# Kernel optimization log

Measured on AMD Instinct MI355X. Metric: run time of the kernel, lower is better.

The kernel has to match this reference:

```python
import jax, jax.numpy as jnp
import numpy as np
import math

B, T, I, H = 16, 16384, 1, 64
OS = 48000.0 / 44100.0  # os_factor


def setup_inputs() -> dict:
    key = jax.random.key(0)
    k0, k1, k2, k3, k4 = jax.random.split(key, 5)
    s = 1.0 / math.sqrt(H)  # torch LSTMCell init range
    x = jax.random.normal(k0, (B, T, I), dtype=jnp.float32)
    W_ih = jax.random.uniform(k1, (4 * H, I), minval=-s, maxval=s, dtype=jnp.float32)
    W_hh = jax.random.uniform(k2, (4 * H, H), minval=-s, maxval=s, dtype=jnp.float32)
    b_ih = jax.random.uniform(k3, (4 * H,), minval=-s, maxval=s, dtype=jnp.float32)
    b_hh = jax.random.uniform(k4, (4 * H,), minval=-s, maxval=s, dtype=jnp.float32)
    return {"x": x, "W_ih": W_ih, "W_hh": W_hh, "b_ih": b_ih, "b_hh": b_hh}


def reference(x, W_ih, W_hh, b_ih, b_hh):
    # allpass fractional-delay parameters (static, os_factor in [1, 2))
    delay_near = math.floor(OS)          # = 1
    alpha = OS - delay_near
    ap_coeff = (1.0 - alpha) / (1.0 + alpha)
    Bsz = x.shape[0]
    S = 2 * H  # LSTM state_size = cat(h, c)

    def lstm_cell(xi, hc):
        h, c = hc[:, :H], hc[:, H:]
        gates = xi @ W_ih.T + b_ih + h @ W_hh.T + b_hh  # [B, 4H]
        ig, fg, gg, og = jnp.split(gates, 4, axis=-1)
        ig = jax.nn.sigmoid(ig)
        fg = jax.nn.sigmoid(fg)
        gg = jnp.tanh(gg)
        og = jax.nn.sigmoid(og)
        c_new = fg * c + ig * gg
        h_new = og * jnp.tanh(c_new)
        return jnp.concatenate([h_new, c_new], axis=-1)  # [B, 2H]

    zeros = jnp.zeros((Bsz, S), dtype=x.dtype)

    def step(carry, xi):
        ap, s1, s2 = carry  # s1 = states[i-1], s2 = states[i-2] (zeros before start)
        ap = ap_coeff * (s1 - ap) + s2
        hc = lstm_cell(xi, ap)
        return (ap, hc, s1), hc

    xs = jnp.swapaxes(x, 0, 1)  # [T, B, I]
    (ap_final, _, _), states = jax.lax.scan(step, (zeros, zeros, zeros), xs)
    states = jnp.swapaxes(states, 0, 1)  # [B, T, 2H]
    y = states[..., :H]
    return y, states[..., H:], ap_final
```

## Files before the change

### kernel.cpp

```cpp
#include <hip/hip_runtime.h>

#define Hdim 64
#define Tlen 16384
#define Bsz  16
#define LOG2E 1.44269504088896340736f

__device__ __forceinline__ float rlane(float v, int l) {
    return __int_as_float(__builtin_amdgcn_readlane(__float_as_int(v), l));
}

__device__ __forceinline__ float sigm(float x) {
    return __builtin_amdgcn_rcpf(1.0f + __builtin_amdgcn_exp2f(-LOG2E * x));
}
__device__ __forceinline__ float tanhfast(float x) {
    const float e = __builtin_amdgcn_exp2f((2.0f * LOG2E) * x);
    return fmaf(-2.0f, __builtin_amdgcn_rcpf(e + 1.0f), 1.0f);
}

__global__ void __launch_bounds__(256, 1)
apdl_rnn_kernel(const float* __restrict__ x,
                const float* __restrict__ W_ih,
                const float* __restrict__ W_hh,
                const float* __restrict__ b_ih,
                const float* __restrict__ b_hh,
                float* __restrict__ out)
{
    const int b    = blockIdx.x;
    const int tid  = threadIdx.x;
    const int wid  = tid >> 6;
    const int lane = tid & 63;

    float w[Hdim];
    #pragma unroll
    for (int k = 0; k < Hdim; k += 4) {
        const float4 v = *reinterpret_cast<const float4*>(&W_hh[tid * Hdim + k]);
        w[k] = v.x; w[k + 1] = v.y; w[k + 2] = v.z; w[k + 3] = v.w;
    }
    const float bias = b_ih[tid] + b_hh[tid];
    const float wih  = W_ih[tid];

    const float apc = 0.8375f;

    float ap_h = 0.f, ap_c = 0.f;
    float h1 = 0.f, c1 = 0.f;
    float h2 = 0.f, c2 = 0.f;

    __shared__ float gbuf[2][256];
    __shared__ float apbuf[4][Hdim];

    const float* xb = x + (size_t)b * Tlen;
    float xnext = xb[lane];
    float xcur  = 0.f;

    float* yp = out + (size_t)b * Tlen * Hdim + lane;
    float* cp = out + (size_t)Bsz * Tlen * Hdim + (size_t)b * Tlen * Hdim + lane;

    float* apw = &apbuf[wid][0];

    for (int t = 0; t < Tlen; ++t) {
        #pragma unroll
        for (int k = 0; k < Hdim; k += 4) {
            asm volatile("" : "+v"(w[k]), "+v"(w[k+1]), "+v"(w[k+2]), "+v"(w[k+3]));
        }

        if ((t & 63) == 0) {
            xcur = xnext;
            if (t + 64 < Tlen) xnext = xb[t + 64 + lane];
        }
        const float xt = rlane(xcur, t & 63);

        ap_h = fmaf(apc, h1 - ap_h, h2);
        ap_c = fmaf(apc, c1 - ap_c, c2);

        apw[lane] = ap_h;

        float a0 = fmaf(xt, wih, bias);
        float a1 = 0.f, a2 = 0.f, a3 = 0.f;
        const float4* hp = reinterpret_cast<const float4*>(apw);
        #pragma unroll
        for (int k4 = 0; k4 < Hdim / 4; ++k4) {
            const float4 hv = hp[k4];
            a0 = fmaf(hv.x, w[4 * k4    ], a0);
            a1 = fmaf(hv.y, w[4 * k4 + 1], a1);
            a2 = fmaf(hv.z, w[4 * k4 + 2], a2);
            a3 = fmaf(hv.w, w[4 * k4 + 3], a3);
        }
        const float gate = (a0 + a1) + (a2 + a3);

        float act;
        if (wid == 2) act = tanhfast(gate);
        else          act = sigm(gate);

        gbuf[t & 1][tid] = act;
        __syncthreads();

        const float* gb = gbuf[t & 1];
        const float ig = gb[lane];
        const float fg = gb[64  + lane];
        const float gg = gb[128 + lane];
        const float og = gb[192 + lane];

        const float cn = fmaf(fg, ap_c, ig * gg);
        const float hn = og * tanhfast(cn);

        h2 = h1; c2 = c1; h1 = hn; c1 = cn;

        if      (wid == 0) *yp = hn;
        else if (wid == 1) *cp = cn;
        yp += Hdim; cp += Hdim;
    }

    if (wid == 0) {
        float* ap_out = out + 2 * (size_t)Bsz * Tlen * Hdim + (size_t)b * 2 * Hdim;
        ap_out[lane]        = ap_h;
        ap_out[Hdim + lane] = ap_c;
    }
}

extern "C" void kernel_launch(void* const* d_in, const int* in_sizes, int n_in,
                              void* d_out, int out_size, void* d_ws, size_t ws_size,
                              hipStream_t stream) {
    const float* x    = (const float*)d_in[0];
    const float* W_ih = (const float*)d_in[1];
    const float* W_hh = (const float*)d_in[2];
    const float* b_ih = (const float*)d_in[3];
    const float* b_hh = (const float*)d_in[4];
    float* out = (float*)d_out;

    apdl_rnn_kernel<<<dim3(Bsz), dim3(256), 0, stream>>>(x, W_ih, W_hh, b_ih, b_hh, out);
}
```

Measured before the change: 10.63 ms.

## Batch all sequences into one block using fp16 MFMA for recurrent matmul

```diff
diff --git a/kernel.cpp b/kernel.cpp
--- a/kernel.cpp
+++ b/kernel.cpp
@@ -5,9 +5,8 @@
 #define Bsz  16
 #define LOG2E 1.44269504088896340736f
 
-__device__ __forceinline__ float rlane(float v, int l) {
-    return __int_as_float(__builtin_amdgcn_readlane(__float_as_int(v), l));
-}
+typedef _Float16 half8 __attribute__((ext_vector_type(8)));
+typedef float    f32x4 __attribute__((ext_vector_type(4)));
 
 __device__ __forceinline__ float sigm(float x) {
     return __builtin_amdgcn_rcpf(1.0f + __builtin_amdgcn_exp2f(-LOG2E * x));
@@ -17,104 +16,137 @@
     return fmaf(-2.0f, __builtin_amdgcn_rcpf(e + 1.0f), 1.0f);
 }
 
-__global__ void __launch_bounds__(256, 1)
-apdl_rnn_kernel(const float* __restrict__ x,
-                const float* __restrict__ W_ih,
-                const float* __restrict__ W_hh,
-                const float* __restrict__ b_ih,
-                const float* __restrict__ b_hh,
-                float* __restrict__ out)
+__global__ void __launch_bounds__(256)
+__attribute__((amdgpu_waves_per_eu(1, 1)))
+apdl_rnn_mfma(const float* __restrict__ x,
+              const float* __restrict__ W_ih,
+              const float* __restrict__ W_hh,
+              const float* __restrict__ b_ih,
+              const float* __restrict__ b_hh,
+              float* __restrict__ out)
 {
-    const int b    = blockIdx.x;
-    const int tid  = threadIdx.x;
-    const int wid  = tid >> 6;
-    const int lane = tid & 63;
+    __shared__ _Float16 wfrag[16 * 2 * 64 * 8];
+    __shared__ char     apraw[2][2048];
+    __shared__ float    xbuf[2][64][16];
+    __shared__ float    bias_lds[256];
+    __shared__ float    wih_lds[256];
 
-    float w[Hdim];
+    const int tid = threadIdx.x;
+    const int w   = tid >> 6;
+    const int l   = tid & 63;
+    const int b   = l & 15;
+    const int g16 = l >> 4;
+    const int j0  = w * 16 + g16 * 4;
+
+    bias_lds[tid] = b_ih[tid] + b_hh[tid];
+    wih_lds[tid]  = W_ih[tid];
+
+    {
+        const int T = tid >> 4, s = tid & 15;
+        #pragma unroll
+        for (int q = 0; q < 4; ++q) {
+            const int vl  = s * 4 + q;
+            const int row = T * 16 + (vl & 15);
+            #pragma unroll
+            for (int c = 0; c < 2; ++c) {
+                const int kb = c * 32 + (vl >> 4) * 8;
+                half8 tmp;
+                #pragma unroll
+                for (int i = 0; i < 8; ++i)
+                    tmp[i] = (_Float16)W_hh[row * 64 + kb + i];
+                *(half8*)&wfrag[((T * 2 + c) * 64 + vl) * 8] = tmp;
+            }
+        }
+    }
+    __syncthreads();
+
+    half8 af[4][2];
+    f32x4 bias4[4], wih4[4];
     #pragma unroll
-    for (int k = 0; k < Hdim; k += 4) {
-        const float4 v = *reinterpret_cast<const float4*>(&W_hh[tid * Hdim + k]);
-        w[k] = v.x; w[k + 1] = v.y; w[k + 2] = v.z; w[k + 3] = v.w;
+    for (int g = 0; g < 4; ++g) {
+        #pragma unroll
+        for (int c = 0; c < 2; ++c)
+            af[g][c] = *(const half8*)&wfrag[(g * 8 + w * 2 + c) * 512 + l * 8];
+        bias4[g] = *(const f32x4*)&bias_lds[g * 64 + j0];
+        wih4[g]  = *(const f32x4*)&wih_lds[g * 64 + j0];
     }
-    const float bias = b_ih[tid] + b_hh[tid];
-    const float wih  = W_ih[tid];
 
-    const float apc = 0.8375f;
+    const int swz     = (b & 7) << 4;
+    const int wr_off  = b * 128 + ((w * 32 + g16 * 8) ^ swz);
+    const int rd0_off = b * 128 + ((g16 * 16) ^ swz);
+    const int rd1_off = b * 128 + ((64 + g16 * 16) ^ swz);
 
-    float ap_h = 0.f, ap_c = 0.f;
-    float h1 = 0.f, c1 = 0.f;
-    float h2 = 0.f, c2 = 0.f;
+    const float apcK = 0.8375f;
+    f32x4 aph = {0,0,0,0}, apcv = {0,0,0,0};
+    f32x4 h1v = {0,0,0,0}, c1v = {0,0,0,0};
+    f32x4 h2v = {0,0,0,0}, c2v = {0,0,0,0};
 
-    __shared__ float gbuf[2][256];
-    __shared__ float apbuf[4][Hdim];
+    float* yp = out + (size_t)b * Tlen * Hdim + j0;
+    float* cp = yp + (size_t)Bsz * Tlen * Hdim;
 
-    const float* xb = x + (size_t)b * Tlen;
-    float xnext = xb[lane];
-    float xcur  = 0.f;
+    const int st_b = tid >> 4;
+    const int st_t = (tid & 15) * 4;
 
-    float* yp = out + (size_t)b * Tlen * Hdim + lane;
-    float* cp = out + (size_t)Bsz * Tlen * Hdim + (size_t)b * Tlen * Hdim + lane;
+    auto step = [&](int t, int par, f32x4& h_prev, f32x4& c_prev,
+                    f32x4& h_prev2, f32x4& c_prev2) {
+        if ((t & 63) == 0) {
+            const int buf = (t >> 6) & 1;
+            const float4 xv = *(const float4*)&x[(size_t)st_b * Tlen + t + st_t];
+            xbuf[buf][st_t + 0][st_b] = xv.x;
+            xbuf[buf][st_t + 1][st_b] = xv.y;
+            xbuf[buf][st_t + 2][st_b] = xv.z;
+            xbuf[buf][st_t + 3][st_b] = xv.w;
+        }
+        #pragma unroll
+        for (int r = 0; r < 4; ++r) {
+            aph[r]  = fmaf(apcK, h_prev[r] - aph[r],  h_prev2[r]);
+            apcv[r] = fmaf(apcK, c_prev[r] - apcv[r], c_prev2[r]);
+        }
+        union { _Float16 h[4]; uint2 u; } pk;
+        #pragma unroll
+        for (int r = 0; r < 4; ++r) pk.h[r] = (_Float16)aph[r];
+        *(uint2*)(apraw[par] + wr_off) = pk.u;
 
-    float* apw = &apbuf[wid][0];
+        __syncthreads();
 
-    for (int t = 0; t < Tlen; ++t) {
+        const float xv  = xbuf[(t >> 6) & 1][t & 63][b];
+        const half8 bf0 = *(const half8*)(apraw[par] + rd0_off);
+        const half8 bf1 = *(const half8*)(apraw[par] + rd1_off);
+
+        f32x4 acc[4];
         #pragma unroll
-        for (int k = 0; k < Hdim; k += 4) {
-            asm volatile("" : "+v"(w[k]), "+v"(w[k+1]), "+v"(w[k+2]), "+v"(w[k+3]));
+        for (int g = 0; g < 4; ++g) {
+            f32x4 ci;
+            #pragma unroll
+            for (int r = 0; r < 4; ++r) ci[r] = fmaf(xv, wih4[g][r], bias4[g][r]);
+            ci     = __builtin_amdgcn_mfma_f32_16x16x32_f16(af[g][0], bf0, ci, 0, 0, 0);
+            acc[g] = __builtin_amdgcn_mfma_f32_16x16x32_f16(af[g][1], bf1, ci, 0, 0, 0);
         }
 
-        if ((t & 63) == 0) {
-            xcur = xnext;
-            if (t + 64 < Tlen) xnext = xb[t + 64 + lane];
+        f32x4 hn, cn;
+        #pragma unroll
+        for (int r = 0; r < 4; ++r) {
+            const float ig = sigm(acc[0][r]);
+            const float fg = sigm(acc[1][r]);
+            const float gg = tanhfast(acc[2][r]);
+            const float og = sigm(acc[3][r]);
+            cn[r] = fmaf(fg, apcv[r], ig * gg);
+            hn[r] = og * tanhfast(cn[r]);
         }
-        const float xt = rlane(xcur, t & 63);
+        *(f32x4*)yp = hn;
+        *(f32x4*)cp = cn;
+        yp += Hdim; cp += Hdim;
+        h_prev2 = hn; c_prev2 = cn;
+    };
 
-        ap_h = fmaf(apc, h1 - ap_h, h2);
-        ap_c = fmaf(apc, c1 - ap_c, c2);
-
-        apw[lane] = ap_h;
-
-        float a0 = fmaf(xt, wih, bias);
-        float a1 = 0.f, a2 = 0.f, a3 = 0.f;
-        const float4* hp = reinterpret_cast<const float4*>(apw);
-        #pragma unroll
-        for (int k4 = 0; k4 < Hdim / 4; ++k4) {
-            const float4 hv = hp[k4];
-            a0 = fmaf(hv.x, w[4 * k4    ], a0);
-            a1 = fmaf(hv.y, w[4 * k4 + 1], a1);
-            a2 = fmaf(hv.z, w[4 * k4 + 2], a2);
-            a3 = fmaf(hv.w, w[4 * k4 + 3], a3);
-        }
-        const float gate = (a0 + a1) + (a2 + a3);
-
-        float act;
-        if (wid == 2) act = tanhfast(gate);
-        else          act = sigm(gate);
-
-        gbuf[t & 1][tid] = act;
-        __syncthreads();
-
-        const float* gb = gbuf[t & 1];
-        const float ig = gb[lane];
-        const float fg = gb[64  + lane];
-        const float gg = gb[128 + lane];
-        const float og = gb[192 + lane];
-
-        const float cn = fmaf(fg, ap_c, ig * gg);
-        const float hn = og * tanhfast(cn);
-
-        h2 = h1; c2 = c1; h1 = hn; c1 = cn;
-
-        if      (wid == 0) *yp = hn;
-        else if (wid == 1) *cp = cn;
-        yp += Hdim; cp += Hdim;
+    for (int t = 0; t < Tlen; t += 2) {
+        step(t,     0, h1v, c1v, h2v, c2v);
+        step(t + 1, 1, h2v, c2v, h1v, c1v);
     }
 
-    if (wid == 0) {
-        float* ap_out = out + 2 * (size_t)Bsz * Tlen * Hdim + (size_t)b * 2 * Hdim;
-        ap_out[lane]        = ap_h;
-        ap_out[Hdim + lane] = ap_c;
-    }
+    float* apf = out + 2 * (size_t)Bsz * Tlen * Hdim + (size_t)b * 2 * Hdim + j0;
+    *(f32x4*)apf          = aph;
+    *(f32x4*)(apf + Hdim) = apcv;
 }
 
 extern "C" void kernel_launch(void* const* d_in, const int* in_sizes, int n_in,
@@ -127,5 +159,5 @@
     const float* b_hh = (const float*)d_in[4];
     float* out = (float*)d_out;
 
-    apdl_rnn_kernel<<<dim3(Bsz), dim3(256), 0, stream>>>(x, W_ih, W_hh, b_ih, b_hh, out);
+    apdl_rnn_mfma<<<dim3(1), dim3(256), 0, stream>>>(x, W_ih, W_hh, b_ih, b_hh, out);
 }
```

After: 8.834 ms. 16.9% less time.
